# Kernel optimization log

Measured on AMD Instinct MI355X. Metric: run time of the kernel, lower is better.

Reference implementation:

```python
import jax, jax.numpy as jnp
import numpy as np


def setup_inputs() -> dict:
    key = jax.random.key(0)
    ks = jax.random.split(key, 6)
    B = 1024
    F, CARD, E = 26, 100, 16          # fields, per-field cardinality (== slice width), emb size
    N_DENSE = 13
    sparse_feat = jax.random.randint(ks[0], (B, F * (CARD + 1)), 0, CARD, dtype=jnp.int64)
    dense_feat = jax.random.normal(ks[1], (B, N_DENSE), dtype=jnp.float32)
    lin_tables = jax.random.normal(ks[2], (F, CARD, 1), dtype=jnp.float32)
    emb_tables = jax.random.normal(ks[3], (F, CARD, E), dtype=jnp.float32)
    linear_w = jax.random.normal(ks[4], (1, F + N_DENSE), dtype=jnp.float32) * 0.1
    linear_b = jax.random.normal(ks[5], (1,), dtype=jnp.float32) * 0.1
    return {"sparse_feat": sparse_feat, "dense_feat": dense_feat,
            "lin_tables": lin_tables, "emb_tables": emb_tables,
            "linear_w": linear_w, "linear_b": linear_b}


def reference(sparse_feat, dense_feat, lin_tables, emb_tables, linear_w, linear_b):
    B = sparse_feat.shape[0]
    F, CARD, E = emb_tables.shape
    # field i occupies columns [i*(CARD+1), i*(CARD+1)+CARD) of sparse_feat
    cols = (jnp.arange(F) * (CARD + 1))[:, None] + jnp.arange(CARD)[None, :]   # [F, CARD]
    idx = sparse_feat[:, cols]                                                  # [B, F, CARD]
    f_idx = jnp.arange(F)[None, :, None]                                        # [1, F, 1]
    # per-field linear-term lookup + sum-pool
    lin = lin_tables[f_idx, idx, 0]                                             # [B, F, CARD]
    sum_lin = jnp.sum(lin, axis=-1)                                             # [B, F]
    lin_in = jnp.concatenate([sum_lin, dense_feat], axis=-1)                    # [B, F+n_dense]
    fm_linear = lin_in @ linear_w.T + linear_b                                  # [B, 1]
    # per-field embedding gather, concat along field axis
    w_x = emb_tables[f_idx, idx]                                                # [B, F, CARD, E]
    w_x = w_x.reshape(B, F * CARD, E)
    # pairwise FM: 0.5 * sum_k[(sum_i x)^2 - sum_i x^2]
    s = jnp.sum(w_x, axis=1)                                                    # [B, E]
    sos = jnp.sum(w_x * w_x, axis=1)                                            # [B, E]
    fm_pairwise = 0.5 * jnp.sum(s * s - sos, axis=-1, keepdims=True)            # [B, 1]
    return fm_linear + fm_pairwise
```

## Files before the change

### kernel.cpp

```cpp
#include <hip/hip_runtime.h>

#define NF     26
#define CARD   100
#define EDIM   16
#define NDENSE 13
#define COLS   2626
#define NLOOK  2600
#define NT     512
#define G      2
#define NQUAD  128
#define MAIN_ITERS 20
#define TAIL_QUADS 40

__global__ __launch_bounds__(NT) void fm_kernel(
    const int*   __restrict__ sparse,
    const float* __restrict__ dense,
    const float* __restrict__ lin_t,
    const float* __restrict__ emb_t,
    const float* __restrict__ lw,
    const float* __restrict__ lb,
    float*       __restrict__ out)
{
    __shared__ unsigned cnt[G * NLOOK];
    __shared__ float    s_w[NF + NDENSE];
    __shared__ float    red[8][G][EDIM + 2];

    const int blk = blockIdx.x;
    const int t   = threadIdx.x;

    for (int i = t; i < G * NLOOK; i += NT) cnt[i] = 0u;
    if (t < NF + NDENSE) s_w[t] = lw[t];
    __syncthreads();

    #pragma unroll
    for (int g = 0; g < G; ++g) {
        const int* row = sparse + (size_t)(G * blk + g) * COLS;
        for (int i = t; i < NLOOK; i += NT) {
            const int f   = i / CARD;
            const int idx = row[i + f];
            atomicAdd(&cnt[g * NLOOK + f * CARD + idx], 1u);
        }
    }
    __syncthreads();

    const int quad = t >> 2;
    const int c    = t & 3;

    float4 s0 = make_float4(0.f, 0.f, 0.f, 0.f);
    float4 s1 = make_float4(0.f, 0.f, 0.f, 0.f);
    float sos0 = 0.f, sos1 = 0.f, lin0 = 0.f, lin1 = 0.f;

    #pragma unroll 5
    for (int i = 0; i < MAIN_ITERS; ++i) {
        const int r = quad + i * NQUAD;
        const float4 v = *reinterpret_cast<const float4*>(emb_t + (r << 4) + (c << 2));
        const float lt  = lin_t[r];
        const int   f   = r / CARD;
        const float lv  = lt * s_w[f];
        const float fc0 = (float)cnt[r];
        const float fc1 = (float)cnt[NLOOK + r];
        const float ssq = v.x*v.x + v.y*v.y + v.z*v.z + v.w*v.w;
        s0.x += fc0 * v.x; s0.y += fc0 * v.y; s0.z += fc0 * v.z; s0.w += fc0 * v.w;
        s1.x += fc1 * v.x; s1.y += fc1 * v.y; s1.z += fc1 * v.z; s1.w += fc1 * v.w;
        sos0 += fc0 * ssq; sos1 += fc1 * ssq;
        lin0 += fc0 * lv;  lin1 += fc1 * lv;
    }
    if (quad < TAIL_QUADS) {
        const int r = quad + MAIN_ITERS * NQUAD;
        const float4 v = *reinterpret_cast<const float4*>(emb_t + (r << 4) + (c << 2));
        const float lt  = lin_t[r];
        const int   f   = r / CARD;
        const float lv  = lt * s_w[f];
        const float fc0 = (float)cnt[r];
        const float fc1 = (float)cnt[NLOOK + r];
        const float ssq = v.x*v.x + v.y*v.y + v.z*v.z + v.w*v.w;
        s0.x += fc0 * v.x; s0.y += fc0 * v.y; s0.z += fc0 * v.z; s0.w += fc0 * v.w;
        s1.x += fc1 * v.x; s1.y += fc1 * v.y; s1.z += fc1 * v.z; s1.w += fc1 * v.w;
        sos0 += fc0 * ssq; sos1 += fc1 * ssq;
        lin0 += fc0 * lv;  lin1 += fc1 * lv;
    }

    #pragma unroll
    for (int off = 32; off >= 4; off >>= 1) {
        s0.x += __shfl_down(s0.x, off, 64); s0.y += __shfl_down(s0.y, off, 64);
        s0.z += __shfl_down(s0.z, off, 64); s0.w += __shfl_down(s0.w, off, 64);
        s1.x += __shfl_down(s1.x, off, 64); s1.y += __shfl_down(s1.y, off, 64);
        s1.z += __shfl_down(s1.z, off, 64); s1.w += __shfl_down(s1.w, off, 64);
        sos0 += __shfl_down(sos0, off, 64); sos1 += __shfl_down(sos1, off, 64);
        lin0 += __shfl_down(lin0, off, 64); lin1 += __shfl_down(lin1, off, 64);
    }
    sos0 += __shfl_down(sos0, 2, 64); sos1 += __shfl_down(sos1, 2, 64);
    lin0 += __shfl_down(lin0, 2, 64); lin1 += __shfl_down(lin1, 2, 64);
    sos0 += __shfl_down(sos0, 1, 64); sos1 += __shfl_down(sos1, 1, 64);
    lin0 += __shfl_down(lin0, 1, 64); lin1 += __shfl_down(lin1, 1, 64);

    const int wave = t >> 6;
    const int lane = t & 63;
    if (lane < 4) {
        red[wave][0][lane*4+0] = s0.x; red[wave][0][lane*4+1] = s0.y;
        red[wave][0][lane*4+2] = s0.z; red[wave][0][lane*4+3] = s0.w;
        red[wave][1][lane*4+0] = s1.x; red[wave][1][lane*4+1] = s1.y;
        red[wave][1][lane*4+2] = s1.z; red[wave][1][lane*4+3] = s1.w;
    }
    if (lane == 0) {
        red[wave][0][EDIM] = sos0; red[wave][0][EDIM+1] = lin0;
        red[wave][1][EDIM] = sos1; red[wave][1][EDIM+1] = lin1;
    }
    __syncthreads();

    if (t < G) {
        const int g = t;
        float pair = 0.f;
        #pragma unroll
        for (int e = 0; e < EDIM; ++e) {
            float fs = 0.f;
            #pragma unroll
            for (int w = 0; w < 8; ++w) fs += red[w][g][e];
            pair += fs * fs;
        }
        float fsos = 0.f, flin = 0.f;
        #pragma unroll
        for (int w = 0; w < 8; ++w) { fsos += red[w][g][EDIM]; flin += red[w][g][EDIM+1]; }
        flin *= 0.25f;
        pair = 0.5f * (pair - fsos);

        const int b = G * blk + g;
        float acc = flin + lb[0];
        const float* drow = dense + (size_t)b * NDENSE;
        #pragma unroll
        for (int dd = 0; dd < NDENSE; ++dd) acc += drow[dd] * s_w[NF + dd];

        out[b] = acc + pair;
    }
}

extern "C" void kernel_launch(void* const* d_in, const int* in_sizes, int n_in,
                              void* d_out, int out_size, void* d_ws, size_t ws_size,
                              hipStream_t stream) {
    const int*   sparse = (const int*)  d_in[0];
    const float* dense  = (const float*)d_in[1];
    const float* lin_t  = (const float*)d_in[2];
    const float* emb_t  = (const float*)d_in[3];
    const float* lw     = (const float*)d_in[4];
    const float* lb     = (const float*)d_in[5];
    float* out = (float*)d_out;

    const int B = out_size;
    fm_kernel<<<B / G, NT, 0, stream>>>(sparse, dense, lin_t, emb_t, lw, lb, out);
}
```

Baseline: 15.66 us.

## Vectorize sparse index loads, precompute linear weights in LDS, prefetch embeddings

```diff
diff --git a/kernel.cpp b/kernel.cpp
--- a/kernel.cpp
+++ b/kernel.cpp
@@ -11,6 +11,7 @@
 #define NQUAD  128
 #define MAIN_ITERS 20
 #define TAIL_QUADS 40
+#define NWAVE  8
 
 __global__ __launch_bounds__(NT) void fm_kernel(
     const int*   __restrict__ sparse,
@@ -22,8 +23,9 @@
     float*       __restrict__ out)
 {
     __shared__ unsigned cnt[G * NLOOK];
+    __shared__ float    lv[NLOOK];
     __shared__ float    s_w[NF + NDENSE];
-    __shared__ float    red[8][G][EDIM + 2];
+    __shared__ float    red[NWAVE][G][EDIM + 2];
 
     const int blk = blockIdx.x;
     const int t   = threadIdx.x;
@@ -32,52 +34,70 @@
     if (t < NF + NDENSE) s_w[t] = lw[t];
     __syncthreads();
 
+    for (int r = t; r < NLOOK; r += NT) {
+        const int f = r / CARD;
+        lv[r] = lin_t[r] * s_w[f];
+    }
+
     #pragma unroll
     for (int g = 0; g < G; ++g) {
         const int* row = sparse + (size_t)(G * blk + g) * COLS;
-        for (int i = t; i < NLOOK; i += NT) {
-            const int f   = i / CARD;
-            const int idx = row[i + f];
-            atomicAdd(&cnt[g * NLOOK + f * CARD + idx], 1u);
+        for (int p = t; p < COLS / 2; p += NT) {
+            const int2 v = reinterpret_cast<const int2*>(row)[p];
+            {
+                const int cc = 2 * p;
+                const int f  = cc / (CARD + 1);
+                const int j  = cc - f * (CARD + 1);
+                if (j < CARD) atomicAdd(&cnt[g * NLOOK + f * CARD + v.x], 1u);
+            }
+            {
+                const int cc = 2 * p + 1;
+                const int f  = cc / (CARD + 1);
+                const int j  = cc - f * (CARD + 1);
+                if (j < CARD) atomicAdd(&cnt[g * NLOOK + f * CARD + v.y], 1u);
+            }
         }
     }
-    __syncthreads();
 
     const int quad = t >> 2;
     const int c    = t & 3;
+    float4 vcur = *reinterpret_cast<const float4*>(emb_t + (quad << 4) + (c << 2));
+
+    __syncthreads();
 
     float4 s0 = make_float4(0.f, 0.f, 0.f, 0.f);
     float4 s1 = make_float4(0.f, 0.f, 0.f, 0.f);
     float sos0 = 0.f, sos1 = 0.f, lin0 = 0.f, lin1 = 0.f;
 
-    #pragma unroll 5
+    #pragma unroll 4
     for (int i = 0; i < MAIN_ITERS; ++i) {
         const int r = quad + i * NQUAD;
+        float4 vnext;
+        if (i + 1 < MAIN_ITERS) {
+            const int rn = quad + (i + 1) * NQUAD;
+            vnext = *reinterpret_cast<const float4*>(emb_t + (rn << 4) + (c << 2));
+        }
+        const float lvr = lv[r];
+        const float fc0 = (float)cnt[r];
+        const float fc1 = (float)cnt[NLOOK + r];
+        const float ssq = vcur.x*vcur.x + vcur.y*vcur.y + vcur.z*vcur.z + vcur.w*vcur.w;
+        s0.x += fc0 * vcur.x; s0.y += fc0 * vcur.y; s0.z += fc0 * vcur.z; s0.w += fc0 * vcur.w;
+        s1.x += fc1 * vcur.x; s1.y += fc1 * vcur.y; s1.z += fc1 * vcur.z; s1.w += fc1 * vcur.w;
+        sos0 += fc0 * ssq; sos1 += fc1 * ssq;
+        lin0 += fc0 * lvr; lin1 += fc1 * lvr;
+        if (i + 1 < MAIN_ITERS) vcur = vnext;
+    }
+    if (quad < TAIL_QUADS) {
+        const int r = quad + MAIN_ITERS * NQUAD;
         const float4 v = *reinterpret_cast<const float4*>(emb_t + (r << 4) + (c << 2));
-        const float lt  = lin_t[r];
-        const int   f   = r / CARD;
-        const float lv  = lt * s_w[f];
+        const float lvr = lv[r];
         const float fc0 = (float)cnt[r];
         const float fc1 = (float)cnt[NLOOK + r];
         const float ssq = v.x*v.x + v.y*v.y + v.z*v.z + v.w*v.w;
         s0.x += fc0 * v.x; s0.y += fc0 * v.y; s0.z += fc0 * v.z; s0.w += fc0 * v.w;
         s1.x += fc1 * v.x; s1.y += fc1 * v.y; s1.z += fc1 * v.z; s1.w += fc1 * v.w;
         sos0 += fc0 * ssq; sos1 += fc1 * ssq;
-        lin0 += fc0 * lv;  lin1 += fc1 * lv;
-    }
-    if (quad < TAIL_QUADS) {
-        const int r = quad + MAIN_ITERS * NQUAD;
-        const float4 v = *reinterpret_cast<const float4*>(emb_t + (r << 4) + (c << 2));
-        const float lt  = lin_t[r];
-        const int   f   = r / CARD;
-        const float lv  = lt * s_w[f];
-        const float fc0 = (float)cnt[r];
-        const float fc1 = (float)cnt[NLOOK + r];
-        const float ssq = v.x*v.x + v.y*v.y + v.z*v.z + v.w*v.w;
-        s0.x += fc0 * v.x; s0.y += fc0 * v.y; s0.z += fc0 * v.z; s0.w += fc0 * v.w;
-        s1.x += fc1 * v.x; s1.y += fc1 * v.y; s1.z += fc1 * v.z; s1.w += fc1 * v.w;
-        sos0 += fc0 * ssq; sos1 += fc1 * ssq;
-        lin0 += fc0 * lv;  lin1 += fc1 * lv;
+        lin0 += fc0 * lvr; lin1 += fc1 * lvr;
     }
 
     #pragma unroll
@@ -115,12 +135,12 @@
         for (int e = 0; e < EDIM; ++e) {
             float fs = 0.f;
             #pragma unroll
-            for (int w = 0; w < 8; ++w) fs += red[w][g][e];
+            for (int w = 0; w < NWAVE; ++w) fs += red[w][g][e];
             pair += fs * fs;
         }
         float fsos = 0.f, flin = 0.f;
         #pragma unroll
-        for (int w = 0; w < 8; ++w) { fsos += red[w][g][EDIM]; flin += red[w][g][EDIM+1]; }
+        for (int w = 0; w < NWAVE; ++w) { fsos += red[w][g][EDIM]; flin += red[w][g][EDIM+1]; }
         flin *= 0.25f;
         pair = 0.5f * (pair - fsos);
 
```

Measured after the change: 15.51 us. About the same (-1.0%).
